# Kernel tuning notes

Measured on AMD Instinct MI355X. Metric: run time of the kernel, lower is better.

## Reference

```python
import jax, jax.numpy as jnp
import numpy as np

D_MODEL = 768
D_FF = 3072
N_HEADS = 12
D_QUART = D_MODEL // 4  # 192
EPS = 1e-5


def layer_norm(x, g, b):
    mu = jnp.mean(x, axis=-1, keepdims=True)
    var = jnp.mean((x - mu) ** 2, axis=-1, keepdims=True)
    return (x - mu) * jax.lax.rsqrt(var + EPS) * g + b


def setup_inputs() -> dict:
    key = jax.random.key(0)
    ks = jax.random.split(key, 24)
    d, dff, dq = D_MODEL, D_FF, D_QUART
    s = lambda k, shape, fan: jax.random.normal(k, shape, jnp.float32) * (1.0 / np.sqrt(fan))
    return {
        "x": jax.random.normal(ks[0], (8, 1024, d), jnp.float32),
        # distance_proj: Linear(1, d//4) -> weight [dq], bias [dq]
        "dp_w": s(ks[1], (dq,), 1), "dp_b": jnp.zeros((dq,), jnp.float32),
        # spatial_encoding: Linear(d,d) GELU Linear(d,d)
        "se_w1": s(ks[2], (d, d), d), "se_b1": jnp.zeros((d,), jnp.float32),
        "se_w2": s(ks[3], (d, d), d), "se_b2": jnp.zeros((d,), jnp.float32),
        # attention projections (stored [in, out])
        "wq": s(ks[4], (d, d), d), "bq": jnp.zeros((d,), jnp.float32),
        "wk": s(ks[5], (d, d), d), "bk": jnp.zeros((d,), jnp.float32),
        "wv": s(ks[6], (d, d), d), "bv": jnp.zeros((d,), jnp.float32),
        "wo": s(ks[7], (d, d), d), "bo": jnp.zeros((d,), jnp.float32),
        # geometric_net FFN
        "gw1": s(ks[8], (d, dff), d), "gb1": jnp.zeros((dff,), jnp.float32),
        "gw2": s(ks[9], (dff, d), dff), "gb2": jnp.zeros((d,), jnp.float32),
        # layer norms
        "n1_g": jnp.ones((d,), jnp.float32), "n1_b": jnp.zeros((d,), jnp.float32),
        "n2_g": jnp.ones((d,), jnp.float32), "n2_b": jnp.zeros((d,), jnp.float32),
    }


def _forward(x, dp_w, dp_b, se_w1, se_b1, se_w2, se_b2,
             wq, bq, wk, bk, wv, bv, wo, bo,
             gw1, gb1, gw2, gb2, n1_g, n1_b, n2_g, n2_b):
    B, N, d = x.shape
    # --- compute_spatial_features ---
    # ||x_i - x_j|| via Gram trick (avoids [B,N,N,d] intermediate)
    sq = jnp.sum(x * x, axis=-1)                      # [B,N]
    gram = jnp.einsum('bnd,bmd->bnm', x, x)           # [B,N,N]
    d2 = jnp.maximum(sq[:, :, None] + sq[:, None, :] - 2.0 * gram, 0.0)
    dist = jnp.sqrt(d2)                               # [B,N,N]
    # Linear(1, d/4) then mean over j commutes: project the mean distance
    mean_d = jnp.mean(dist, axis=2)                   # [B,N]
    spat = mean_d[..., None] * dp_w + dp_b            # [B,N,d/4]
    spat = jnp.pad(spat, ((0, 0), (0, 0), (0, d - D_QUART)))  # [B,N,d]
    # spatial_encoding MLP (exact GELU, matching torch nn.GELU default)
    h = jax.nn.gelu(spat @ se_w1 + se_b1, approximate=False)
    x = x + (h @ se_w2 + se_b2)
    # --- attention block ---
    res = x
    xn = layer_norm(x, n1_g, n1_b)
    H, dh = N_HEADS, d // N_HEADS
    q = (xn @ wq + bq).reshape(B, N, H, dh)
    k = (xn @ wk + bk).reshape(B, N, H, dh)
    v = (xn @ wv + bv).reshape(B, N, H, dh)
    scores = jnp.einsum('bqhd,bkhd->bhqk', q, k) / np.sqrt(dh)
    attn = jax.nn.softmax(scores, axis=-1)
    o = jnp.einsum('bhqk,bkhd->bqhd', attn, v).reshape(B, N, d)
    x = res + (o @ wo + bo)
    # --- FFN block ---
    res = x
    xn = layer_norm(x, n2_g, n2_b)
    h = jax.nn.gelu(xn @ gw1 + gb1, approximate=False)
    x = res + (h @ gw2 + gb2)
    return x


def reference(x, dp_w, dp_b, se_w1, se_b1, se_w2, se_b2,
              wq, bq, wk, bk, wv, bv, wo, bo,
              gw1, gb1, gw2, gb2, n1_g, n1_b, n2_g, n2_b):
    return _forward(x, dp_w, dp_b, se_w1, se_b1, se_w2, se_b2,
                    wq, bq, wk, bk, wv, bv, wo, bo,
                    gw1, gb1, gw2, gb2, n1_g, n1_b, n2_g, n2_b)
```

## Files before the change

### kernel.cpp

```cpp
#include <hip/hip_runtime.h>
#include <hip/hip_bf16.h>

typedef unsigned short ushort;
typedef __attribute__((ext_vector_type(8))) __bf16 bf16x8;
typedef __attribute__((ext_vector_type(4))) float f32x4;
typedef __attribute__((ext_vector_type(8))) ushort ushort8;

__device__ inline ushort f2bf(float f) {
    union { float f; unsigned u; } a{f};
    unsigned r = a.u + 0x7FFFu + ((a.u >> 16) & 1u);
    return (ushort)(r >> 16);
}
__device__ inline float gelu_f(float x) {
    return 0.5f * x * (1.f + erff(x * 0.70710678118654752f));
}

__global__ void transpose_to_bf16(const float* __restrict__ Wm, ushort* __restrict__ Wt, int K, int N) {
    __shared__ float tile[32][33];
    int k0 = blockIdx.x * 32, n0 = blockIdx.y * 32;
    int tx = threadIdx.x, ty = threadIdx.y;
    #pragma unroll
    for (int r = ty; r < 32; r += 8) tile[r][tx] = Wm[(size_t)(k0 + r) * N + n0 + tx];
    __syncthreads();
    #pragma unroll
    for (int r = ty; r < 32; r += 8) Wt[(size_t)(n0 + r) * K + k0 + tx] = f2bf(tile[tx][r]);
}

__global__ void rowstat(const float* __restrict__ x, ushort* __restrict__ xb, float* __restrict__ sq) {
    int row = blockIdx.x;
    const float* xr = x + (size_t)row * 768;
    ushort* xbr = xb + (size_t)row * 768;
    int t = threadIdx.x;
    float s = 0.f;
    #pragma unroll
    for (int i = 0; i < 3; ++i) {
        float vv = xr[t + i * 256];
        xbr[t + i * 256] = f2bf(vv);
        s += vv * vv;
    }
    #pragma unroll
    for (int off = 1; off < 64; off <<= 1) s += __shfl_xor(s, off);
    __shared__ float wsum[4];
    if ((t & 63) == 0) wsum[t >> 6] = s;
    __syncthreads();
    if (t == 0) sq[row] = wsum[0] + wsum[1] + wsum[2] + wsum[3];
}

__global__ void precomp_ac(const float* __restrict__ dp_w, const float* __restrict__ dp_b,
                           const float* __restrict__ se_w1, const float* __restrict__ se_b1,
                           float* __restrict__ Avec, float* __restrict__ Cvec) {
    int o = blockIdx.x * 256 + threadIdx.x;
    float a = 0.f, c = 0.f;
    for (int i = 0; i < 192; ++i) {
        float w = se_w1[(size_t)i * 768 + o];
        a += dp_w[i] * w;
        c += dp_b[i] * w;
    }
    Avec[o] = a;
    Cvec[o] = c + se_b1[o];
}

__global__ void hgen(const float* __restrict__ mean_acc, const float* __restrict__ Avec,
                     const float* __restrict__ Cvec, ushort* __restrict__ h) {
    int row = blockIdx.x;
    float md = mean_acc[row] * (1.f / 1024.f);
    int t = threadIdx.x;
    #pragma unroll
    for (int i = 0; i < 3; ++i) {
        int o = t + i * 256;
        h[(size_t)row * 768 + o] = f2bf(gelu_f(md * Avec[o] + Cvec[o]));
    }
}

__global__ void lnorm(const float* __restrict__ xin, const float* __restrict__ g,
                      const float* __restrict__ b, ushort* __restrict__ xn) {
    int row = blockIdx.x;
    const float* xr = xin + (size_t)row * 768;
    int t = threadIdx.x;
    float v[3];
    float s = 0.f, s2 = 0.f;
    #pragma unroll
    for (int i = 0; i < 3; ++i) {
        v[i] = xr[t + i * 256];
        s += v[i];
        s2 += v[i] * v[i];
    }
    #pragma unroll
    for (int off = 1; off < 64; off <<= 1) { s += __shfl_xor(s, off); s2 += __shfl_xor(s2, off); }
    __shared__ float a0[4], a1[4];
    if ((t & 63) == 0) { a0[t >> 6] = s; a1[t >> 6] = s2; }
    __syncthreads();
    s = a0[0] + a0[1] + a0[2] + a0[3];
    s2 = a1[0] + a1[1] + a1[2] + a1[3];
    float mu = s * (1.f / 768.f);
    float var = s2 * (1.f / 768.f) - mu * mu;
    float rs = rsqrtf(var + 1e-5f);
    #pragma unroll
    for (int i = 0; i < 3; ++i) {
        int o = t + i * 256;
        xn[(size_t)row * 768 + o] = f2bf((v[i] - mu) * rs * g[o] + b[o]);
    }
}

#define BM 128
#define BK 32

enum { EPI_BF16 = 0, EPI_GELU = 1, EPI_RES = 2, EPI_GRAM = 3, EPI_QKV = 4 };

template <int EPI, int BNT>
__launch_bounds__(256, BNT == 64 ? 4 : 2)
__global__ void gemm_bt(const ushort* __restrict__ A, const ushort* __restrict__ Bt,
                        int M, int N, int K,
                        const float* __restrict__ bias,
                        const float* res, float* outf,
                        ushort* __restrict__ outh,
                        const float* __restrict__ sq, float* __restrict__ mean_acc) {
    __shared__ __align__(16) ushort As[2][BM * BK];
    __shared__ __align__(16) ushort Bs[2][BNT * BK];

    unsigned gx = gridDim.x, gy = gridDim.y;
    unsigned flat = blockIdx.x + gx * (blockIdx.y + gy * blockIdx.z);
    unsigned total = gx * gy * gridDim.z;
    unsigned chunk = total >> 3;
    flat = (flat & 7) * chunk + (flat >> 3);
    unsigned bx = flat % gx;
    unsigned rem = flat / gx;
    unsigned by = rem % gy;
    unsigned bz = rem / gy;

    int m0 = bx * BM;
    int n0 = by * BNT;
    if (EPI == EPI_GRAM) {
        A += (size_t)bz * 1024 * 768;
        Bt = A;
        sq += bz * 1024;
        mean_acc += bz * 1024;
    }
    int t = threadIdx.x, w = t >> 6, l = t & 63;
    int lg = l >> 4, li = l & 15;
    constexpr int MI = (BNT == 128) ? 4 : 2;
    int wm = (BNT == 128) ? (w >> 1) * 64 : w * 32;
    int wn = (BNT == 128) ? (w & 1) * 64 : 0;

    int srow = l >> 2, scol = (l & 3) * 8;
    const ushort* agp0 = A + (size_t)(m0 + (2 * w) * 16 + srow) * K + scol;
    const ushort* agp1 = A + (size_t)(m0 + (2 * w + 1) * 16 + srow) * K + scol;
    const ushort* bgp0;
    const ushort* bgp1 = nullptr;
    ushort* la0 = &As[0][(2 * w) * 16 * BK];
    ushort* lb0;
    if (BNT == 128) {
        bgp0 = Bt + (size_t)(n0 + (2 * w) * 16 + srow) * K + scol;
        bgp1 = Bt + (size_t)(n0 + (2 * w + 1) * 16 + srow) * K + scol;
        lb0 = &Bs[0][(2 * w) * 16 * BK];
    } else {
        bgp0 = Bt + (size_t)(n0 + w * 16 + srow) * K + scol;
        lb0 = &Bs[0][w * 16 * BK];
    }

    f32x4 acc[MI][4] = {};

    auto stage = [&](int buf, int kt) {
        size_t ko = (size_t)kt * BK;
        ushort* la = la0 + buf * (BM * BK);
        ushort* lb = lb0 + buf * (BNT * BK);
        __builtin_amdgcn_global_load_lds((const __attribute__((address_space(1))) void*)(agp0 + ko),
                                         (__attribute__((address_space(3))) void*)la, 16, 0, 0);
        __builtin_amdgcn_global_load_lds((const __attribute__((address_space(1))) void*)(agp1 + ko),
                                         (__attribute__((address_space(3))) void*)(la + 16 * BK), 16, 0, 0);
        __builtin_amdgcn_global_load_lds((const __attribute__((address_space(1))) void*)(bgp0 + ko),
                                         (__attribute__((address_space(3))) void*)lb, 16, 0, 0);
        if (BNT == 128)
            __builtin_amdgcn_global_load_lds((const __attribute__((address_space(1))) void*)(bgp1 + ko),
                                             (__attribute__((address_space(3))) void*)(lb + 16 * BK), 16, 0, 0);
    };

    int nk = K / BK;
    stage(0, 0);
    __syncthreads();
    int buf = 0;
    for (int kt = 0; kt < nk; ++kt) {
        if (kt + 1 < nk) stage(buf ^ 1, kt + 1);
        bf16x8 af[MI], bfr[4];
        #pragma unroll
        for (int i = 0; i < MI; ++i)
            af[i] = *reinterpret_cast<const bf16x8*>(&As[buf][(wm + i * 16 + li) * BK + lg * 8]);
        #pragma unroll
        for (int i = 0; i < 4; ++i)
            bfr[i] = *reinterpret_cast<const bf16x8*>(&Bs[buf][(wn + i * 16 + li) * BK + lg * 8]);
        #pragma unroll
        for (int mi = 0; mi < MI; ++mi)
            #pragma unroll
            for (int ni = 0; ni < 4; ++ni)
                acc[mi][ni] = __builtin_amdgcn_mfma_f32_16x16x32_bf16(af[mi], bfr[ni], acc[mi][ni], 0, 0, 0);
        __syncthreads();
        buf ^= 1;
    }

    #pragma unroll
    for (int mi = 0; mi < MI; ++mi) {
        #pragma unroll
        for (int r = 0; r < 4; ++r) {
            int row = m0 + wm + mi * 16 + lg * 4 + r;
            if (EPI == EPI_GRAM) {
                float si = sq[row];
                float s = 0.f;
                #pragma unroll
                for (int ni = 0; ni < 4; ++ni) {
                    int col = n0 + wn + ni * 16 + li;
                    float d2 = si + sq[col] - 2.f * acc[mi][ni][r];
                    s += sqrtf(fmaxf(d2, 0.f));
                }
                s += __shfl_xor(s, 1); s += __shfl_xor(s, 2);
                s += __shfl_xor(s, 4); s += __shfl_xor(s, 8);
                if (li == 0) atomicAdd(&mean_acc[row], s);
            } else {
                #pragma unroll
                for (int ni = 0; ni < 4; ++ni) {
                    int col = n0 + wn + ni * 16 + li;
                    float v = acc[mi][ni][r] + bias[col];
                    if (EPI == EPI_BF16) outh[(size_t)row * N + col] = f2bf(v);
                    if (EPI == EPI_GELU) outh[(size_t)row * N + col] = f2bf(gelu_f(v));
                    if (EPI == EPI_RES) outf[(size_t)row * N + col] = res[(size_t)row * N + col] + v;
                    if (EPI == EPI_QKV) {
                        int which = col / 768;
                        int c2 = col - which * 768;
                        outh[(size_t)which * (8192 * 768) + (size_t)row * 768 + c2] = f2bf(v);
                    }
                }
            }
        }
    }
}

template <int EPI>
__launch_bounds__(512, 4)
__global__ void gemm8(const ushort* __restrict__ A, const ushort* __restrict__ Bt,
                      int M, int N, int K,
                      const float* __restrict__ bias,
                      const float* res, float* outf, ushort* __restrict__ outh) {
    __shared__ __align__(16) ushort As[3][2][128 * 32];
    __shared__ __align__(16) ushort Bs[3][128 * 32];

    unsigned gx = gridDim.x;
    unsigned orig = blockIdx.x + gx * blockIdx.y;
    unsigned xcd = orig & 7;
    unsigned q = orig >> 3;
    unsigned mpg = gx >> 3;
    unsigned mloc = q % mpg;
    unsigned n = q / mpg;
    int m0 = (xcd * mpg + mloc) * 256;
    int n0 = n * 128;

    int t = threadIdx.x, w = t >> 6, l = t & 63;
    int lg = l >> 4, li = l & 15;
    int wr = w >> 1, wc = w & 1;
    int ha = wr >> 1;
    int ra = (wr & 1) * 64;

    f32x4 acc[4][4] = {};

    auto stage = [&](int buf, int kt) {
        int k0 = kt * 32;
        int d = w * 1024 + l * 16;
        int dp = d ^ ((((d >> 6) ^ (d >> 8)) & 3) << 4);
        int srow = dp >> 6, scol = (dp & 63) >> 1;
        #pragma unroll
        for (int h = 0; h < 2; ++h) {
            const ushort* src = A + (size_t)(m0 + h * 128 + srow) * K + k0 + scol;
            __builtin_amdgcn_global_load_lds(
                (const __attribute__((address_space(1))) void*)src,
                (__attribute__((address_space(3))) void*)&As[buf][h][w * 512], 16, 0, 0);
        }
        {
            const ushort* src = Bt + (size_t)(n0 + srow) * K + k0 + scol;
            __builtin_amdgcn_global_load_lds(
                (const __attribute__((address_space(1))) void*)src,
                (__attribute__((address_space(3))) void*)&Bs[buf][w * 512], 16, 0, 0);
        }
    };

    int nk = K / 32;
    stage(0, 0);
    stage(1, 1);
    stage(2, 2);
    for (int kt = 0; kt < nk; ++kt) {
        int buf = kt % 3;
        if (kt + 2 < nk)      asm volatile("s_waitcnt vmcnt(6)" ::: "memory");
        else if (kt + 1 < nk) asm volatile("s_waitcnt vmcnt(3)" ::: "memory");
        else                  asm volatile("s_waitcnt vmcnt(0)" ::: "memory");
        asm volatile("s_barrier" ::: "memory");
        __builtin_amdgcn_sched_barrier(0);
        bf16x8 af[4], bf[4];
        #pragma unroll
        for (int mi = 0; mi < 4; ++mi) {
            int e = (ra + mi * 16 + li) * 64 + lg * 16;
            int ep = e ^ ((((e >> 6) ^ (e >> 8)) & 3) << 4);
            af[mi] = *reinterpret_cast<const bf16x8*>((const char*)&As[buf][ha][0] + ep);
        }
        #pragma unroll
        for (int ni = 0; ni < 4; ++ni) {
            int e = (wc * 64 + ni * 16 + li) * 64 + lg * 16;
            int ep = e ^ ((((e >> 6) ^ (e >> 8)) & 3) << 4);
            bf[ni] = *reinterpret_cast<const bf16x8*>((const char*)&Bs[buf][0] + ep);
        }
        __builtin_amdgcn_s_setprio(1);
        #pragma unroll
        for (int mi = 0; mi < 4; ++mi)
            #pragma unroll
            for (int ni = 0; ni < 4; ++ni)
                acc[mi][ni] = __builtin_amdgcn_mfma_f32_16x16x32_bf16(af[mi], bf[ni], acc[mi][ni], 0, 0, 0);
        __builtin_amdgcn_s_setprio(0);
        asm volatile("s_barrier" ::: "memory");
        __builtin_amdgcn_sched_barrier(0);
        if (kt + 3 < nk) stage(buf, kt + 3);
    }

    #pragma unroll
    for (int mi = 0; mi < 4; ++mi) {
        #pragma unroll
        for (int r = 0; r < 4; ++r) {
            int row = m0 + wr * 64 + mi * 16 + lg * 4 + r;
            #pragma unroll
            for (int ni = 0; ni < 4; ++ni) {
                int col = n0 + wc * 64 + ni * 16 + li;
                float v = acc[mi][ni][r] + bias[col];
                if (EPI == EPI_GELU) outh[(size_t)row * N + col] = f2bf(gelu_f(v));
                if (EPI == EPI_RES)  outf[(size_t)row * N + col] = res[(size_t)row * N + col] + v;
                if (EPI == EPI_QKV) {
                    int which = col / 768;
                    int c2 = col - which * 768;
                    outh[(size_t)which * (8192 * 768) + (size_t)row * 768 + c2] = f2bf(v);
                }
            }
        }
    }
}

__launch_bounds__(256, 3)
__global__ void flash_attn(const ushort* __restrict__ q, const ushort* __restrict__ k,
                           const ushort* __restrict__ v, ushort* __restrict__ o) {
    int flat = blockIdx.x + 8 * (blockIdx.y + 12 * blockIdx.z);
    flat = (flat & 7) * 96 + (flat >> 3);
    int qt = flat & 7;
    int rem = flat >> 3;
    int h = rem % 12;
    int b = rem / 12;

    int t = threadIdx.x, w = t >> 6, l = t & 63;
    int lg = l >> 4, li = l & 15;

    __shared__ __align__(16) ushort Vt[2][64][72];
    __shared__ __align__(16) ushort P[4][32][72];

    const size_t hoff = (size_t)h * 64;
    const size_t bbase = (size_t)b * 1024 * 768;

    bf16x8 qf[2][2];
    #pragma unroll
    for (int f = 0; f < 2; ++f) {
        int qrow = qt * 128 + w * 32 + f * 16 + li;
        const ushort* qp = &q[bbase + (size_t)qrow * 768 + hoff];
        qf[f][0] = *reinterpret_cast<const bf16x8*>(qp + lg * 8);
        qf[f][1] = *reinterpret_cast<const bf16x8*>(qp + 32 + lg * 8);
    }

    bf16x8 onesf;
    #pragma unroll
    for (int i = 0; i < 8; ++i) onesf[i] = (__bf16)1.0f;

    float m_[2][4];
    f32x4 oacc[2][4];
    f32x4 oell[2];
    #pragma unroll
    for (int f = 0; f < 2; ++f) {
        #pragma unroll
        for (int r = 0; r < 4; ++r) m_[f][r] = -1e30f;
        oell[f] = f32x4{0.f, 0.f, 0.f, 0.f};
        #pragma unroll
        for (int n = 0; n < 4; ++n) oacc[f][n] = f32x4{0.f, 0.f, 0.f, 0.f};
    }

    int vrow = t & 63;
    int vc = t >> 6;
    const ushort* vbase = &v[bbase + hoff];

    ushort8 vv0 = *reinterpret_cast<const ushort8*>(&vbase[(size_t)vrow * 768 + vc * 8]);
    ushort8 vv1 = *reinterpret_cast<const ushort8*>(&vbase[(size_t)vrow * 768 + (vc + 4) * 8]);

    for (int jt = 0; jt < 16; ++jt) {
        int j0 = jt * 64, buf = jt & 1;
        #pragma unroll
        for (int i = 0; i < 8; ++i) Vt[buf][vc * 8 + i][vrow] = vv0[i];
        #pragma unroll
        for (int i = 0; i < 8; ++i) Vt[buf][(vc + 4) * 8 + i][vrow] = vv1[i];
        if (jt < 15) {
            vv0 = *reinterpret_cast<const ushort8*>(&vbase[(size_t)(j0 + 64 + vrow) * 768 + vc * 8]);
            vv1 = *reinterpret_cast<const ushort8*>(&vbase[(size_t)(j0 + 64 + vrow) * 768 + (vc + 4) * 8]);
        }
        bf16x8 kf0[4], kf1[4];
        #pragma unroll
        for (int jj = 0; jj < 4; ++jj) {
            const ushort* kp = &k[bbase + (size_t)(j0 + jj * 16 + li) * 768 + hoff];
            kf0[jj] = *reinterpret_cast<const bf16x8*>(kp + lg * 8);
            kf1[jj] = *reinterpret_cast<const bf16x8*>(kp + 32 + lg * 8);
        }
        f32x4 s[2][4];
        #pragma unroll
        for (int jj = 0; jj < 4; ++jj)
            #pragma unroll
            for (int f = 0; f < 2; ++f) {
                f32x4 a = {0.f, 0.f, 0.f, 0.f};
                a = __builtin_amdgcn_mfma_f32_16x16x32_bf16(qf[f][0], kf0[jj], a, 0, 0, 0);
                a = __builtin_amdgcn_mfma_f32_16x16x32_bf16(qf[f][1], kf1[jj], a, 0, 0, 0);
                s[f][jj] = a * 0.125f;
            }
        #pragma unroll
        for (int f = 0; f < 2; ++f) {
            float mt[4];
            #pragma unroll
            for (int r = 0; r < 4; ++r)
                mt[r] = fmaxf(fmaxf(s[f][0][r], s[f][1][r]), fmaxf(s[f][2][r], s[f][3][r]));
            #pragma unroll
            for (int r = 0; r < 4; ++r) {
                mt[r] = fmaxf(mt[r], __shfl_xor(mt[r], 1));
                mt[r] = fmaxf(mt[r], __shfl_xor(mt[r], 2));
                mt[r] = fmaxf(mt[r], __shfl_xor(mt[r], 4));
                mt[r] = fmaxf(mt[r], __shfl_xor(mt[r], 8));
            }
            bool need = (mt[0] > m_[f][0] + 8.f) | (mt[1] > m_[f][1] + 8.f) |
                        (mt[2] > m_[f][2] + 8.f) | (mt[3] > m_[f][3] + 8.f);
            if (__any(need)) {
                #pragma unroll
                for (int r = 0; r < 4; ++r) {
                    float mn = fmaxf(m_[f][r], mt[r]);
                    float al = __expf(m_[f][r] - mn);
                    m_[f][r] = mn;
                    #pragma unroll
                    for (int n = 0; n < 4; ++n) oacc[f][n][r] *= al;
                    oell[f][r] *= al;
                }
            }
            #pragma unroll
            for (int jj = 0; jj < 4; ++jj)
                #pragma unroll
                for (int r = 0; r < 4; ++r)
                    P[w][f * 16 + lg * 4 + r][jj * 16 + li] = f2bf(__expf(s[f][jj][r] - m_[f][r]));
        }
        __syncthreads();
        bf16x8 pf[2][2];
        #pragma unroll
        for (int f = 0; f < 2; ++f) {
            pf[f][0] = *reinterpret_cast<const bf16x8*>(&P[w][f * 16 + li][lg * 8]);
            pf[f][1] = *reinterpret_cast<const bf16x8*>(&P[w][f * 16 + li][32 + lg * 8]);
        }
        #pragma unroll
        for (int f = 0; f < 2; ++f) {
            oell[f] = __builtin_amdgcn_mfma_f32_16x16x32_bf16(pf[f][0], onesf, oell[f], 0, 0, 0);
            oell[f] = __builtin_amdgcn_mfma_f32_16x16x32_bf16(pf[f][1], onesf, oell[f], 0, 0, 0);
        }
        #pragma unroll
        for (int n = 0; n < 4; ++n) {
            bf16x8 vf0 = *reinterpret_cast<const bf16x8*>(&Vt[buf][n * 16 + li][lg * 8]);
            bf16x8 vf1 = *reinterpret_cast<const bf16x8*>(&Vt[buf][n * 16 + li][32 + lg * 8]);
            #pragma unroll
            for (int f = 0; f < 2; ++f) {
                oacc[f][n] = __builtin_amdgcn_mfma_f32_16x16x32_bf16(pf[f][0], vf0, oacc[f][n], 0, 0, 0);
                oacc[f][n] = __builtin_amdgcn_mfma_f32_16x16x32_bf16(pf[f][1], vf1, oacc[f][n], 0, 0, 0);
            }
        }
    }
    #pragma unroll
    for (int f = 0; f < 2; ++f)
        #pragma unroll
        for (int n = 0; n < 4; ++n)
            #pragma unroll
            for (int r = 0; r < 4; ++r) {
                int row = qt * 128 + w * 32 + f * 16 + lg * 4 + r;
                o[bbase + (size_t)row * 768 + hoff + n * 16 + li] = f2bf(oacc[f][n][r] / oell[f][r]);
            }
}

extern "C" void kernel_launch(void* const* d_in, const int* in_sizes, int n_in,
                              void* d_out, int out_size, void* d_ws, size_t ws_size,
                              hipStream_t stream) {
    const float* x = (const float*)d_in[0];
    const float* dp_w = (const float*)d_in[1];
    const float* dp_b = (const float*)d_in[2];
    const float* se_w1 = (const float*)d_in[3];
    const float* se_b1 = (const float*)d_in[4];
    const float* se_w2 = (const float*)d_in[5];
    const float* se_b2 = (const float*)d_in[6];
    const float* wq = (const float*)d_in[7];  const float* bq = (const float*)d_in[8];
    const float* wk = (const float*)d_in[9];  const float* bk = (const float*)d_in[10];
    const float* wv = (const float*)d_in[11]; const float* bv = (const float*)d_in[12];
    const float* wo = (const float*)d_in[13]; const float* bo = (const float*)d_in[14];
    const float* gw1 = (const float*)d_in[15]; const float* gb1 = (const float*)d_in[16];
    const float* gw2 = (const float*)d_in[17]; const float* gb2 = (const float*)d_in[18];
    const float* n1g = (const float*)d_in[19]; const float* n1b = (const float*)d_in[20];
    const float* n2g = (const float*)d_in[21]; const float* n2b = (const float*)d_in[22];
    float* out = (float*)d_out;

    constexpr size_t SZ_ACT = (size_t)8192 * 768 * 2;
    char* W = (char*)d_ws;
    ushort* xb = (ushort*)(W);
    ushort* q_ = (ushort*)(W + SZ_ACT);
    ushort* k_ = (ushort*)(W + 2 * SZ_ACT);
    ushort* v_ = (ushort*)(W + 3 * SZ_ACT);
    ushort* o_ = (ushort*)(W + 4 * SZ_ACT);
    ushort* hsp = q_;
    ushort* hff = q_;
    ushort* wqt = (ushort*)(W + 5 * SZ_ACT);
    ushort* wkt = wqt + (size_t)768 * 768;
    ushort* wvt = wkt + (size_t)768 * 768;
    ushort* wot = wvt + (size_t)768 * 768;
    ushort* sw2t = wot + (size_t)768 * 768;
    ushort* g1t = sw2t + (size_t)768 * 768;
    ushort* g2t = g1t + (size_t)768 * 3072;
    float* sqv = (float*)(g2t + (size_t)3072 * 768);
    float* meanv = sqv + 8192;
    float* Avec = meanv + 8192;
    float* Cvec = Avec + 768;
    float* bqkv = Cvec + 768;

    dim3 tb(32, 8);
    transpose_to_bf16<<<dim3(24, 24), tb, 0, stream>>>(se_w2, sw2t, 768, 768);
    transpose_to_bf16<<<dim3(24, 24), tb, 0, stream>>>(wq, wqt, 768, 768);
    transpose_to_bf16<<<dim3(24, 24), tb, 0, stream>>>(wk, wkt, 768, 768);
    transpose_to_bf16<<<dim3(24, 24), tb, 0, stream>>>(wv, wvt, 768, 768);
    transpose_to_bf16<<<dim3(24, 24), tb, 0, stream>>>(wo, wot, 768, 768);
    transpose_to_bf16<<<dim3(24, 96), tb, 0, stream>>>(gw1, g1t, 768, 3072);
    transpose_to_bf16<<<dim3(96, 24), tb, 0, stream>>>(gw2, g2t, 3072, 768);
    hipMemcpyAsync(bqkv, bq, 768 * sizeof(float), hipMemcpyDeviceToDevice, stream);
    hipMemcpyAsync(bqkv + 768, bk, 768 * sizeof(float), hipMemcpyDeviceToDevice, stream);
    hipMemcpyAsync(bqkv + 1536, bv, 768 * sizeof(float), hipMemcpyDeviceToDevice, stream);

    rowstat<<<8192, 256, 0, stream>>>(x, xb, sqv);
    precomp_ac<<<3, 256, 0, stream>>>(dp_w, dp_b, se_w1, se_b1, Avec, Cvec);
    hipMemsetAsync(meanv, 0, 8192 * sizeof(float), stream);

    gemm_bt<EPI_GRAM, 128><<<dim3(8, 8, 8), 256, 0, stream>>>(xb, xb, 1024, 1024, 768,
                                                              nullptr, nullptr, nullptr, nullptr, sqv, meanv);
    hgen<<<8192, 256, 0, stream>>>(meanv, Avec, Cvec, hsp);
    gemm8<EPI_RES><<<dim3(32, 6), 512, 0, stream>>>(hsp, sw2t, 8192, 768, 768,
                                                    se_b2, x, out, nullptr);
    lnorm<<<8192, 256, 0, stream>>>(out, n1g, n1b, xb);
    gemm8<EPI_QKV><<<dim3(32, 18), 512, 0, stream>>>(xb, wqt, 8192, 2304, 768,
                                                     bqkv, nullptr, nullptr, q_);
    flash_attn<<<dim3(8, 12, 8), 256, 0, stream>>>(q_, k_, v_, o_);
    gemm8<EPI_RES><<<dim3(32, 6), 512, 0, stream>>>(o_, wot, 8192, 768, 768,
                                                    bo, out, out, nullptr);
    lnorm<<<8192, 256, 0, stream>>>(out, n2g, n2b, xb);
    gemm8<EPI_GELU><<<dim3(32, 24), 512, 0, stream>>>(xb, g1t, 8192, 3072, 768,
                                                      gb1, nullptr, nullptr, hff);
    gemm8<EPI_RES><<<dim3(32, 6), 512, 0, stream>>>(hff, g2t, 8192, 768, 3072,
                                                    gb2, out, out, nullptr);
}
```

Before: 472.8 us.

## Replace 256x128 triple-buffered GEMM with 128x128 double-buffered tiles plus split-K FFN2

The 512-thread, 256x128-tile, triple-buffered GEMM with swizzled LDS is replaced by a 256-thread 128x128-tile double-buffered kernel without swizzle. The grid doubles in M, and the final FFN down-projection uses split-K=2 with atomicAdd into the output. The flash attention MFMA sections also get s_setprio hints. The smaller tiles and split-K add parallelism and occupancy. The costs are more bank conflicts from the unswizzled LDS layout, a shallower pipeline that issues each prefetch in the same iteration that consumes the previous buffer, atomic traffic, and non-deterministic summation order.

```diff
diff --git a/kernel.cpp b/kernel.cpp
--- a/kernel.cpp
+++ b/kernel.cpp
@@ -105,7 +105,7 @@
 #define BM 128
 #define BK 32
 
-enum { EPI_BF16 = 0, EPI_GELU = 1, EPI_RES = 2, EPI_GRAM = 3, EPI_QKV = 4 };
+enum { EPI_BF16 = 0, EPI_GELU = 1, EPI_RES = 2, EPI_GRAM = 3, EPI_QKV = 4, EPI_RESK = 5 };
 
 template <int EPI, int BNT>
 __launch_bounds__(256, BNT == 64 ? 4 : 2)
@@ -234,103 +234,97 @@
 }
 
 template <int EPI>
-__launch_bounds__(512, 4)
-__global__ void gemm8(const ushort* __restrict__ A, const ushort* __restrict__ Bt,
+__launch_bounds__(256, 3)
+__global__ void gemm4(const ushort* __restrict__ A, const ushort* __restrict__ Bt,
                       int M, int N, int K,
                       const float* __restrict__ bias,
                       const float* res, float* outf, ushort* __restrict__ outh) {
-    __shared__ __align__(16) ushort As[3][2][128 * 32];
-    __shared__ __align__(16) ushort Bs[3][128 * 32];
-
-    unsigned gx = gridDim.x;
-    unsigned orig = blockIdx.x + gx * blockIdx.y;
+    __shared__ __align__(16) ushort As[2][128 * 32];
+    __shared__ __align__(16) ushort Bs[2][128 * 32];
+
+    unsigned gx = gridDim.x, gy = gridDim.y;
+    unsigned orig = blockIdx.x + gx * (blockIdx.y + gy * blockIdx.z);
     unsigned xcd = orig & 7;
     unsigned q = orig >> 3;
     unsigned mpg = gx >> 3;
     unsigned mloc = q % mpg;
-    unsigned n = q / mpg;
-    int m0 = (xcd * mpg + mloc) * 256;
+    unsigned rest = q / mpg;
+    unsigned n = rest % gy;
+    unsigned split = rest / gy;
+    int m0 = (xcd * mpg + mloc) * 128;
     int n0 = n * 128;
+    int Keff = (EPI == EPI_RESK) ? (K >> 1) : K;
+    int kbase = (EPI == EPI_RESK) ? (int)split * Keff : 0;
 
     int t = threadIdx.x, w = t >> 6, l = t & 63;
     int lg = l >> 4, li = l & 15;
-    int wr = w >> 1, wc = w & 1;
-    int ha = wr >> 1;
-    int ra = (wr & 1) * 64;
+    int wm = (w >> 1) * 64, wn = (w & 1) * 64;
+
+    int srow = l >> 2, scol = (l & 3) * 8;
+    const ushort* agp0 = A + (size_t)(m0 + (2 * w) * 16 + srow) * K + kbase + scol;
+    const ushort* agp1 = A + (size_t)(m0 + (2 * w + 1) * 16 + srow) * K + kbase + scol;
+    const ushort* bgp0 = Bt + (size_t)(n0 + (2 * w) * 16 + srow) * K + kbase + scol;
+    const ushort* bgp1 = Bt + (size_t)(n0 + (2 * w + 1) * 16 + srow) * K + kbase + scol;
+    ushort* la0 = &As[0][(2 * w) * 16 * 32];
+    ushort* lb0 = &Bs[0][(2 * w) * 16 * 32];
 
     f32x4 acc[4][4] = {};
 
     auto stage = [&](int buf, int kt) {
-        int k0 = kt * 32;
-        int d = w * 1024 + l * 16;
-        int dp = d ^ ((((d >> 6) ^ (d >> 8)) & 3) << 4);
-        int srow = dp >> 6, scol = (dp & 63) >> 1;
-        #pragma unroll
-        for (int h = 0; h < 2; ++h) {
-            const ushort* src = A + (size_t)(m0 + h * 128 + srow) * K + k0 + scol;
-            __builtin_amdgcn_global_load_lds(
-                (const __attribute__((address_space(1))) void*)src,
-                (__attribute__((address_space(3))) void*)&As[buf][h][w * 512], 16, 0, 0);
-        }
-        {
-            const ushort* src = Bt + (size_t)(n0 + srow) * K + k0 + scol;
-            __builtin_amdgcn_global_load_lds(
-                (const __attribute__((address_space(1))) void*)src,
-                (__attribute__((address_space(3))) void*)&Bs[buf][w * 512], 16, 0, 0);
-        }
+        size_t ko = (size_t)kt * 32;
+        ushort* la = la0 + buf * (128 * 32);
+        ushort* lb = lb0 + buf * (128 * 32);
+        __builtin_amdgcn_global_load_lds((const __attribute__((address_space(1))) void*)(agp0 + ko),
+                                         (__attribute__((address_space(3))) void*)la, 16, 0, 0);
+        __builtin_amdgcn_global_load_lds((const __attribute__((address_space(1))) void*)(agp1 + ko),
+                                         (__attribute__((address_space(3))) void*)(la + 16 * 32), 16, 0, 0);
+        __builtin_amdgcn_global_load_lds((const __attribute__((address_space(1))) void*)(bgp0 + ko),
+                                         (__attribute__((address_space(3))) void*)lb, 16, 0, 0);
+        __builtin_amdgcn_global_load_lds((const __attribute__((address_space(1))) void*)(bgp1 + ko),
+                                         (__attribute__((address_space(3))) void*)(lb + 16 * 32), 16, 0, 0);
     };
 
-    int nk = K / 32;
+    int nk = Keff / 32;
     stage(0, 0);
-    stage(1, 1);
-    stage(2, 2);
+    __syncthreads();
+    int buf = 0;
     for (int kt = 0; kt < nk; ++kt) {
-        int buf = kt % 3;
-        if (kt + 2 < nk)      asm volatile("s_waitcnt vmcnt(6)" ::: "memory");
-        else if (kt + 1 < nk) asm volatile("s_waitcnt vmcnt(3)" ::: "memory");
-        else                  asm volatile("s_waitcnt vmcnt(0)" ::: "memory");
-        asm volatile("s_barrier" ::: "memory");
-        __builtin_amdgcn_sched_barrier(0);
-        bf16x8 af[4], bf[4];
-        #pragma unroll
-        for (int mi = 0; mi < 4; ++mi) {
-            int e = (ra + mi * 16 + li) * 64 + lg * 16;
-            int ep = e ^ ((((e >> 6) ^ (e >> 8)) & 3) << 4);
-            af[mi] = *reinterpret_cast<const bf16x8*>((const char*)&As[buf][ha][0] + ep);
-        }
-        #pragma unroll
-        for (int ni = 0; ni < 4; ++ni) {
-            int e = (wc * 64 + ni * 16 + li) * 64 + lg * 16;
-            int ep = e ^ ((((e >> 6) ^ (e >> 8)) & 3) << 4);
-            bf[ni] = *reinterpret_cast<const bf16x8*>((const char*)&Bs[buf][0] + ep);
-        }
-        __builtin_amdgcn_s_setprio(1);
+        if (kt + 1 < nk) stage(buf ^ 1, kt + 1);
+        bf16x8 af[4], bfr[4];
+        #pragma unroll
+        for (int i = 0; i < 4; ++i) {
+            af[i] = *reinterpret_cast<const bf16x8*>(&As[buf][(wm + i * 16 + li) * 32 + lg * 8]);
+            bfr[i] = *reinterpret_cast<const bf16x8*>(&Bs[buf][(wn + i * 16 + li) * 32 + lg * 8]);
+        }
         #pragma unroll
         for (int mi = 0; mi < 4; ++mi)
             #pragma unroll
             for (int ni = 0; ni < 4; ++ni)
-                acc[mi][ni] = __builtin_amdgcn_mfma_f32_16x16x32_bf16(af[mi], bf[ni], acc[mi][ni], 0, 0, 0);
-        __builtin_amdgcn_s_setprio(0);
-        asm volatile("s_barrier" ::: "memory");
-        __builtin_amdgcn_sched_barrier(0);
-        if (kt + 3 < nk) stage(buf, kt + 3);
+                acc[mi][ni] = __builtin_amdgcn_mfma_f32_16x16x32_bf16(af[mi], bfr[ni], acc[mi][ni], 0, 0, 0);
+        __syncthreads();
+        buf ^= 1;
     }
 
     #pragma unroll
     for (int mi = 0; mi < 4; ++mi) {
         #pragma unroll
         for (int r = 0; r < 4; ++r) {
-            int row = m0 + wr * 64 + mi * 16 + lg * 4 + r;
+            int row = m0 + wm + mi * 16 + lg * 4 + r;
             #pragma unroll
             for (int ni = 0; ni < 4; ++ni) {
-                int col = n0 + wc * 64 + ni * 16 + li;
-                float v = acc[mi][ni][r] + bias[col];
-                if (EPI == EPI_GELU) outh[(size_t)row * N + col] = f2bf(gelu_f(v));
-                if (EPI == EPI_RES)  outf[(size_t)row * N + col] = res[(size_t)row * N + col] + v;
-                if (EPI == EPI_QKV) {
-                    int which = col / 768;
-                    int c2 = col - which * 768;
-                    outh[(size_t)which * (8192 * 768) + (size_t)row * 768 + c2] = f2bf(v);
+                int col = n0 + wn + ni * 16 + li;
+                if (EPI == EPI_RESK) {
+                    float v = acc[mi][ni][r] + (split == 0 ? bias[col] : 0.f);
+                    atomicAdd(&outf[(size_t)row * N + col], v);
+                } else {
+                    float v = acc[mi][ni][r] + bias[col];
+                    if (EPI == EPI_GELU) outh[(size_t)row * N + col] = f2bf(gelu_f(v));
+                    if (EPI == EPI_RES)  outf[(size_t)row * N + col] = res[(size_t)row * N + col] + v;
+                    if (EPI == EPI_QKV) {
+                        int which = col / 768;
+                        int c2 = col - which * 768;
+                        outh[(size_t)which * (8192 * 768) + (size_t)row * 768 + c2] = f2bf(v);
+                    }
                 }
             }
         }
@@ -406,6 +400,7 @@
             kf1[jj] = *reinterpret_cast<const bf16x8*>(kp + 32 + lg * 8);
         }
         f32x4 s[2][4];
+        __builtin_amdgcn_s_setprio(1);
         #pragma unroll
         for (int jj = 0; jj < 4; ++jj)
             #pragma unroll
@@ -415,6 +410,7 @@
                 a = __builtin_amdgcn_mfma_f32_16x16x32_bf16(qf[f][1], kf1[jj], a, 0, 0, 0);
                 s[f][jj] = a * 0.125f;
             }
+        __builtin_amdgcn_s_setprio(0);
         #pragma unroll
         for (int f = 0; f < 2; ++f) {
             float mt[4];
@@ -454,6 +450,7 @@
             pf[f][0] = *reinterpret_cast<const bf16x8*>(&P[w][f * 16 + li][lg * 8]);
             pf[f][1] = *reinterpret_cast<const bf16x8*>(&P[w][f * 16 + li][32 + lg * 8]);
         }
+        __builtin_amdgcn_s_setprio(1);
         #pragma unroll
         for (int f = 0; f < 2; ++f) {
             oell[f] = __builtin_amdgcn_mfma_f32_16x16x32_bf16(pf[f][0], onesf, oell[f], 0, 0, 0);
@@ -469,6 +466,7 @@
                 oacc[f][n] = __builtin_amdgcn_mfma_f32_16x16x32_bf16(pf[f][1], vf1, oacc[f][n], 0, 0, 0);
             }
         }
+        __builtin_amdgcn_s_setprio(0);
     }
     #pragma unroll
     for (int f = 0; f < 2; ++f)
@@ -542,17 +540,17 @@
     gemm_bt<EPI_GRAM, 128><<<dim3(8, 8, 8), 256, 0, stream>>>(xb, xb, 1024, 1024, 768,
                                                               nullptr, nullptr, nullptr, nullptr, sqv, meanv);
     hgen<<<8192, 256, 0, stream>>>(meanv, Avec, Cvec, hsp);
-    gemm8<EPI_RES><<<dim3(32, 6), 512, 0, stream>>>(hsp, sw2t, 8192, 768, 768,
+    gemm4<EPI_RES><<<dim3(64, 6), 256, 0, stream>>>(hsp, sw2t, 8192, 768, 768,
                                                     se_b2, x, out, nullptr);
     lnorm<<<8192, 256, 0, stream>>>(out, n1g, n1b, xb);
-    gemm8<EPI_QKV><<<dim3(32, 18), 512, 0, stream>>>(xb, wqt, 8192, 2304, 768,
+    gemm4<EPI_QKV><<<dim3(64, 18), 256, 0, stream>>>(xb, wqt, 8192, 2304, 768,
                                                      bqkv, nullptr, nullptr, q_);
     flash_attn<<<dim3(8, 12, 8), 256, 0, stream>>>(q_, k_, v_, o_);
-    gemm8<EPI_RES><<<dim3(32, 6), 512, 0, stream>>>(o_, wot, 8192, 768, 768,
+    gemm4<EPI_RES><<<dim3(64, 6), 256, 0, stream>>>(o_, wot, 8192, 768, 768,
                                                     bo, out, out, nullptr);
     lnorm<<<8192, 256, 0, stream>>>(out, n2g, n2b, xb);
-    gemm8<EPI_GELU><<<dim3(32, 24), 512, 0, stream>>>(xb, g1t, 8192, 3072, 768,
+    gemm4<EPI_GELU><<<dim3(64, 24), 256, 0, stream>>>(xb, g1t, 8192, 3072, 768,
                                                       gb1, nullptr, nullptr, hff);
-    gemm8<EPI_RES><<<dim3(32, 6), 512, 0, stream>>>(hff, g2t, 8192, 768, 3072,
-                                                    gb2, out, out, nullptr);
-}
+    gemm4<EPI_RESK><<<dim3(64, 6, 2), 256, 0, stream>>>(hff, g2t, 8192, 768, 3072,
+                                                        gb2, nullptr, out, nullptr);
+}
```

Result: faster. 429.9 us (-9.1%).
